# Kernel tuning notes

Hardware: AMD Instinct MI355X
Metric: run time of the kernel (lower is better)

Reference implementation:

```python
import jax, jax.numpy as jnp
import numpy as np

N_ATOMS = 512
NC2 = N_ATOMS * (N_ATOMS - 1) // 2  # 130816
BATCH = 512

# Static strictly-lower-triangular indices (i > j), row-major order of (i, j),
# which matches tf.where's row-major enumeration of nonzero entries of
# band_part(c,-1,0) - band_part(c,0,0).
_TRI_I, _TRI_J = np.tril_indices(N_ATOMS, k=-1)
TRI_I = jnp.asarray(_TRI_I, dtype=jnp.int32)
TRI_J = jnp.asarray(_TRI_J, dtype=jnp.int32)


def setup_inputs() -> dict:
    key = jax.random.key(0)
    atom_nc = jax.random.normal(key, (BATCH, N_ATOMS), dtype=jnp.float32)
    return {"atom_nc": atom_nc}


def reference(atom_nc):
    # c[b, i, j] = nc[b, i] * nc[b, j]; keep strictly-lower-triangular entries
    # (i > j) flattened row-major -> [B, NC2]. Computed directly via static
    # gathered pair indices (same math as the dense outer product + mask +
    # dynamic where/gather in the original, assuming nonzero charges).
    return atom_nc[:, TRI_I] * atom_nc[:, TRI_J]
```

## Files before the change

### kernel.cpp

```cpp
#include <hip/hip_runtime.h>


#define N_ATOMS 512
#define NC2     130816
#define NQ4     (NC2 / 4)
#define GX      8
#define NITER   16

__device__ __forceinline__ int skew(int t) { return t + (t >> 5); }

__global__ __launch_bounds__(256, 8)
void ncp_kernel(const float* __restrict__ in, float* __restrict__ out) {
    __shared__ float row[N_ATOMS + (N_ATOMS >> 5) + 8];
    const int b   = blockIdx.y;
    const int tid = threadIdx.x;

    {
        const float2* src = reinterpret_cast<const float2*>(in + (size_t)b * N_ATOMS);
        float2 v = src[tid];
        const int t = 2 * tid;
        row[skew(t)]     = v.x;
        row[skew(t) + 1] = v.y;
    }
    __syncthreads();

    float4* outb = reinterpret_cast<float4*>(out + (size_t)b * NC2);
    const int q0 = blockIdx.x * 256 + tid;

#pragma unroll 4
    for (int s = 0; s < NITER; ++s) {
        const int q = q0 + s * (GX * 256);
        if (q < NQ4) {
            const int k = q * 4;

            int i  = (int)(0.5f * (1.0f + sqrtf(8.0f * (float)k + 1.0f)));
            int t2 = (i * (i - 1)) >> 1;
            if (t2 > k)           { t2 -= --i; }
            else if (k >= t2 + i) { t2 += i++; }
            int j = k - t2;

            float ri = row[skew(i)];
            float4 v;
            float* vp = &v.x;
#pragma unroll
            for (int t = 0; t < 4; ++t) {
                vp[t] = ri * row[skew(j)];
                ++j; bool c = (j == i); i += c; j = c ? 0 : j; ri = row[skew(i)];
            }
            outb[q] = v;
        }
    }
}

extern "C" void kernel_launch(void* const* d_in, const int* in_sizes, int n_in,
                              void* d_out, int out_size, void* d_ws, size_t ws_size,
                              hipStream_t stream) {
    const float* atom_nc = (const float*)d_in[0];
    float* out = (float*)d_out;

    dim3 grid(GX, 512);
    dim3 block(256);
    ncp_kernel<<<grid, block, 0, stream>>>(atom_nc, out);
}
```

Baseline: 47.20 us.

## Use one 1024-thread block per batch row with unguarded full iterations

Changes the work split so that each batch row is handled by a single 1024-thread block instead of 8 blocks of 256 threads. The row is then staged into shared memory once per row rather than once per block, and the loop runs a fixed count of full iterations with no bounds check, plus one guarded tail pass. The cost is a grid of only 512 large blocks, so fewer independent blocks are available to balance load across CUs. The launch bound of 8 blocks of 1024 threads per SM may also be unattainable.

After: 46.22 us. 2.1% less time.

```diff
diff --git a/kernel.cpp b/kernel.cpp
--- a/kernel.cpp
+++ b/kernel.cpp
@@ -4,51 +4,51 @@
 #define N_ATOMS 512
 #define NC2     130816
 #define NQ4     (NC2 / 4)
-#define GX      8
-#define NITER   16
+#define BLK     1024
+#define NFULL   (NQ4 / BLK)
+#define NTAIL   (NQ4 - NFULL * BLK)
 
 __device__ __forceinline__ int skew(int t) { return t + (t >> 5); }
 
-__global__ __launch_bounds__(256, 8)
+__device__ __forceinline__ void do_quad(const float* __restrict__ row,
+                                        float4* __restrict__ outb, int q) {
+    const int k = q * 4;
+    int i  = (int)(0.5f * (1.0f + sqrtf(8.0f * (float)k + 1.0f)));
+    int t2 = (i * (i - 1)) >> 1;
+    if (t2 > k)           { t2 -= --i; }
+    else if (k >= t2 + i) { t2 += i++; }
+    int j = k - t2;
+
+    float ri = row[skew(i)];
+    float4 v;
+    float* vp = &v.x;
+#pragma unroll
+    for (int t = 0; t < 4; ++t) {
+        vp[t] = ri * row[skew(j)];
+        ++j; bool c = (j == i); i += c; j = c ? 0 : j; ri = row[skew(i)];
+    }
+    outb[q] = v;
+}
+
+__global__ __launch_bounds__(BLK, 8)
 void ncp_kernel(const float* __restrict__ in, float* __restrict__ out) {
     __shared__ float row[N_ATOMS + (N_ATOMS >> 5) + 8];
-    const int b   = blockIdx.y;
+    const int b   = blockIdx.x;
     const int tid = threadIdx.x;
 
-    {
-        const float2* src = reinterpret_cast<const float2*>(in + (size_t)b * N_ATOMS);
-        float2 v = src[tid];
-        const int t = 2 * tid;
-        row[skew(t)]     = v.x;
-        row[skew(t) + 1] = v.y;
+    if (tid < N_ATOMS) {
+        row[skew(tid)] = in[(size_t)b * N_ATOMS + tid];
     }
     __syncthreads();
 
     float4* outb = reinterpret_cast<float4*>(out + (size_t)b * NC2);
-    const int q0 = blockIdx.x * 256 + tid;
 
 #pragma unroll 4
-    for (int s = 0; s < NITER; ++s) {
-        const int q = q0 + s * (GX * 256);
-        if (q < NQ4) {
-            const int k = q * 4;
-
-            int i  = (int)(0.5f * (1.0f + sqrtf(8.0f * (float)k + 1.0f)));
-            int t2 = (i * (i - 1)) >> 1;
-            if (t2 > k)           { t2 -= --i; }
-            else if (k >= t2 + i) { t2 += i++; }
-            int j = k - t2;
-
-            float ri = row[skew(i)];
-            float4 v;
-            float* vp = &v.x;
-#pragma unroll
-            for (int t = 0; t < 4; ++t) {
-                vp[t] = ri * row[skew(j)];
-                ++j; bool c = (j == i); i += c; j = c ? 0 : j; ri = row[skew(i)];
-            }
-            outb[q] = v;
-        }
+    for (int s = 0; s < NFULL; ++s) {
+        do_quad(row, outb, s * BLK + tid);
+    }
+    if (tid < NTAIL) {
+        do_quad(row, outb, NFULL * BLK + tid);
     }
 }
 
@@ -58,7 +58,7 @@
     const float* atom_nc = (const float*)d_in[0];
     float* out = (float*)d_out;
 
-    dim3 grid(GX, 512);
-    dim3 block(256);
+    dim3 grid(512);
+    dim3 block(BLK);
     ncp_kernel<<<grid, block, 0, stream>>>(atom_nc, out);
 }
```
